# Performance work log

Measured on AMD Instinct MI355X. Metric: run time of the kernel, lower is better.

Reference implementation:

```python
import jax, jax.numpy as jnp
import numpy as np

N_NODES = 50000
N_EDGES = 1600000


def gcn_conv(x, edge_index, W, b):
    """PyG GCNConv: linear transform, add self-loops, symmetric deg^-1/2 norm, scatter-add."""
    n = x.shape[0]
    h = x @ W  # [N, out]
    loop = jnp.arange(n)
    src = jnp.concatenate([edge_index[0], loop])
    dst = jnp.concatenate([edge_index[1], loop])
    ones = jnp.ones(src.shape[0], dtype=h.dtype)
    deg = jax.ops.segment_sum(ones, dst, num_segments=n)  # in-degree incl. self-loop
    dinv = jnp.where(deg > 0, jax.lax.rsqrt(deg), 0.0)
    norm = dinv[src] * dinv[dst]  # [E+N]
    msg = h[src] * norm[:, None]  # gathered, normalized messages
    out = jax.ops.segment_sum(msg, dst, num_segments=n)
    return out + b


def setup_inputs() -> dict:
    key = jax.random.key(0)
    k1, k2, k3, k4 = jax.random.split(key, 4)
    x = jax.random.normal(k1, (N_NODES, 512), dtype=jnp.float32)
    edge_index = jax.random.randint(k2, (2, N_EDGES), 0, N_NODES, dtype=jnp.int64)
    W1 = jax.random.normal(k3, (512, 128), dtype=jnp.float32) * (1.0 / np.sqrt(512))
    b1 = jnp.zeros((128,), dtype=jnp.float32)
    W2 = jax.random.normal(k4, (128, 40), dtype=jnp.float32) * (1.0 / np.sqrt(128))
    b2 = jnp.zeros((40,), dtype=jnp.float32)
    return {"x": x, "edge_index": edge_index, "W1": W1, "b1": b1, "W2": W2, "b2": b2}


def reference(x, edge_index, W1, b1, W2, b2):
    h = gcn_conv(x, edge_index, W1, b1)
    h = jax.nn.relu(h)
    h = gcn_conv(h, edge_index, W2, b2)
    return jax.nn.log_softmax(h, axis=1)
```

## Files before the change

kernel.cpp:

```cpp
#include <hip/hip_runtime.h>
#include <hip/hip_bf16.h>
#include <math.h>


#define FEAT1 512
#define FEAT2 128
#define FEAT3 40

typedef __attribute__((ext_vector_type(8))) short bf16x8;
typedef __attribute__((ext_vector_type(4))) float f32x4;

struct __align__(16) ll2 { long long x, y; };

__device__ __forceinline__ unsigned short f2bf(float f) {
    union { float f; unsigned u; } c; c.f = f;
    unsigned r = c.u + 0x7fff + ((c.u >> 16) & 1);
    return (unsigned short)(r >> 16);
}
__device__ __forceinline__ float bf2f(unsigned v16) {
    union { unsigned u; float f; } c; c.u = v16 << 16;
    return c.f;
}

__device__ __forceinline__ bf16x8 pack_bf8(f32x4 a, f32x4 b) {
    union { __hip_bfloat162 h[4]; bf16x8 v; } u;
    u.h[0] = __float22bfloat162_rn(make_float2(a[0], a[1]));
    u.h[1] = __float22bfloat162_rn(make_float2(a[2], a[3]));
    u.h[2] = __float22bfloat162_rn(make_float2(b[0], b[1]));
    u.h[3] = __float22bfloat162_rn(make_float2(b[2], b[3]));
    return u.v;
}

__launch_bounds__(1024)
__global__ void partA_kernel(const int* __restrict__ ei,
                             int* __restrict__ gbkt, unsigned* __restrict__ part,
                             int bktCap, long E, int NB) {
    __shared__ int hist[256], lbase[256], lcur[256];
    __shared__ int anyv;
    int t = threadIdx.x;
    if (t == 0) anyv = 0;
    if (t < 256) { hist[t] = 0; lcur[t] = 0; }
    __syncthreads();
    if (t < 256 && ei[2 * t + 1] != 0) anyv = 1;
    __syncthreads();
    int f64 = (anyv == 0) ? 1 : 0;
    const long long* ei64 = (const long long*)ei;
    bool al4 = ((E & 3) == 0);

    long chunk = (E + gridDim.x - 1) / gridDim.x;
    chunk = (chunk + 3) & ~3L;
    long start = (long)blockIdx.x * chunk;
    long end = start + chunk; if (end > E) end = E;
    if (start > E) start = E;

    int srcs[8], dsts[8];
    #pragma unroll
    for (int r = 0; r < 2; r++) {
        long e0 = start + (long)r * 4096 + 4 * t;
        if (al4 && e0 + 3 < end) {
            if (f64) {
                ll2 sa = *(const ll2*)(ei64 + e0);
                ll2 sb = *(const ll2*)(ei64 + e0 + 2);
                ll2 da = *(const ll2*)(ei64 + E + e0);
                ll2 db = *(const ll2*)(ei64 + E + e0 + 2);
                srcs[4 * r + 0] = (int)sa.x; srcs[4 * r + 1] = (int)sa.y;
                srcs[4 * r + 2] = (int)sb.x; srcs[4 * r + 3] = (int)sb.y;
                dsts[4 * r + 0] = (int)da.x; dsts[4 * r + 1] = (int)da.y;
                dsts[4 * r + 2] = (int)db.x; dsts[4 * r + 3] = (int)db.y;
            } else {
                int4 s4 = *(const int4*)(ei + e0);
                int4 d4 = *(const int4*)(ei + E + e0);
                srcs[4 * r + 0] = s4.x; srcs[4 * r + 1] = s4.y;
                srcs[4 * r + 2] = s4.z; srcs[4 * r + 3] = s4.w;
                dsts[4 * r + 0] = d4.x; dsts[4 * r + 1] = d4.y;
                dsts[4 * r + 2] = d4.z; dsts[4 * r + 3] = d4.w;
            }
            #pragma unroll
            for (int u = 0; u < 4; u++) atomicAdd(&hist[dsts[4 * r + u] >> 8], 1);
        } else {
            #pragma unroll
            for (int u = 0; u < 4; u++) {
                if (e0 + u < end) {
                    if (f64) { srcs[4 * r + u] = (int)ei64[e0 + u]; dsts[4 * r + u] = (int)ei64[E + e0 + u]; }
                    else     { srcs[4 * r + u] = ei[e0 + u];        dsts[4 * r + u] = ei[E + e0 + u]; }
                    atomicAdd(&hist[dsts[4 * r + u] >> 8], 1);
                }
            }
        }
    }
    __syncthreads();
    if (t < NB && hist[t]) lbase[t] = atomicAdd(&gbkt[t], hist[t]);
    __syncthreads();

    #pragma unroll
    for (int r = 0; r < 2; r++) {
        long e0 = start + (long)r * 4096 + 4 * t;
        #pragma unroll
        for (int u = 0; u < 4; u++) {
            if (e0 + u < end) {
                int bkt = dsts[4 * r + u] >> 8;
                int pos = lbase[bkt] + atomicAdd(&lcur[bkt], 1);
                if (pos < bktCap)
                    part[(long)bkt * bktCap + pos] =
                        (unsigned)srcs[4 * r + u] | ((unsigned)(dsts[4 * r + u] & 255) << 17);
            }
        }
    }
}

__launch_bounds__(512)
__global__ void partB_kernel(const unsigned* __restrict__ part, int bktCap,
                             const int* __restrict__ gbkt,
                             int* __restrict__ offsets, float* __restrict__ dinv,
                             int* __restrict__ col, int N, int E) {
    __shared__ int h[256], sc[256], cur[256];
    int b = blockIdx.x, t = threadIdx.x;
    int NB = gridDim.x;

    if (t < 256) sc[t] = (t < NB) ? gbkt[t] : 0;
    __syncthreads();
    #pragma unroll
    for (int d = 1; d < 256; d <<= 1) {
        int tv = 0;
        if (t < 256 && t >= d) tv = sc[t - d];
        __syncthreads();
        if (t < 256) sc[t] += tv;
        __syncthreads();
    }
    int base = (b == 0) ? 0 : sc[b - 1];
    if (b == 0 && t == 0) offsets[N] = E;

    int n = gbkt[b]; if (n > bktCap) n = bktCap;
    int lo = b << 8;
    const unsigned* p = part + (long)b * bktCap;
    if (t < 256) h[t] = 0;
    __syncthreads();
    for (int i = t; i < n; i += 512) atomicAdd(&h[(p[i] >> 17) & 255], 1);
    __syncthreads();
    int cnt = (t < 256) ? h[t] : 0;
    if (t < 256) sc[t] = cnt;
    __syncthreads();
    #pragma unroll
    for (int d = 1; d < 256; d <<= 1) {
        int tv = 0;
        if (t < 256 && t >= d) tv = sc[t - d];
        __syncthreads();
        if (t < 256) sc[t] += tv;
        __syncthreads();
    }
    if (t < 256) {
        int ex = sc[t] - cnt;
        int node = lo + t;
        if (node < N) {
            offsets[node] = base + ex;
            dinv[node] = 1.0f / sqrtf((float)(cnt + 1));
        }
        cur[t] = ex;
    }
    __syncthreads();
    for (int i = t; i < n; i += 512) {
        unsigned u = p[i];
        int r = atomicAdd(&cur[(u >> 17) & 255], 1);
        col[base + r] = u & 0x1FFFF;
    }
}

__global__ void wbt_kernel(const float* __restrict__ W1, const float* __restrict__ W2,
                           unsigned short* __restrict__ Bt, unsigned short* __restrict__ Bt2,
                           int* __restrict__ gbkt) {
    int b = blockIdx.x;
    if (b == 0 && threadIdx.x < 256) gbkt[threadIdx.x] = 0;
    if (b < FEAT2) {
        int r = b, x7 = r & 7;
        for (int k = threadIdx.x; k < FEAT1; k += blockDim.x) {
            int c = k >> 3, j = k & 7;
            int eo = (((c ^ x7) << 3) | j);
            Bt[(long)r * FEAT1 + eo] = f2bf(W1[(long)k * FEAT2 + r]);
        }
    } else {
        int n = b - FEAT2;
        for (int k = threadIdx.x; k < FEAT2; k += blockDim.x)
            Bt2[(long)n * FEAT2 + k] = (n < FEAT3) ? f2bf(W2[(long)k * FEAT3 + n]) : 0;
    }
}

#define G1_NW 8
__launch_bounds__(512, 2)
__global__ void gemm1_mfma_kernel(const float* __restrict__ A,
                                  const unsigned short* __restrict__ Bsw,
                                  const float* __restrict__ dinv,
                                  unsigned short* __restrict__ C, int M) {
    __shared__ unsigned short Bl[FEAT2 * FEAT1];
    int t = threadIdx.x;

    {
        uint4 tmp[16];
        #pragma unroll
        for (int r = 0; r < 16; r++)
            tmp[r] = *(const uint4*)((const char*)Bsw + (size_t)t * 16 + (size_t)r * 8192);
        #pragma unroll
        for (int r = 0; r < 16; r++)
            *(uint4*)((char*)Bl + (size_t)t * 16 + (size_t)r * 8192) = tmp[r];
    }
    __syncthreads();

    int w = t >> 6, lane = t & 63;
    int quad = lane >> 4, r15 = lane & 15;
    int row0 = (blockIdx.x * (G1_NW * 2) + w * 2) * 16;
    int x7 = r15 & 7;

    int ar0 = row0 + r15;      if (ar0 >= M) ar0 = M - 1;
    int ar1 = row0 + 16 + r15; if (ar1 >= M) ar1 = M - 1;
    const float* ap0 = A + (long)ar0 * FEAT1 + quad * 8;
    const float* ap1 = A + (long)ar1 * FEAT1 + quad * 8;

    f32x4 ra0[3][2], ra1[3][2];
    #pragma unroll
    for (int p = 0; p < 3; p++) {
        ra0[p][0] = *(const f32x4*)(ap0 + p * 32);
        ra0[p][1] = *(const f32x4*)(ap0 + p * 32 + 4);
        ra1[p][0] = *(const f32x4*)(ap1 + p * 32);
        ra1[p][1] = *(const f32x4*)(ap1 + p * 32 + 4);
    }

    f32x4 acc0[8], acc1[8];
    #pragma unroll
    for (int nt = 0; nt < 8; nt++) {
        acc0[nt] = (f32x4){0.f, 0.f, 0.f, 0.f};
        acc1[nt] = (f32x4){0.f, 0.f, 0.f, 0.f};
    }

    #pragma unroll
    for (int ks = 0; ks < 16; ks++) {
        int sl = ks % 3;
        bf16x8 af0 = pack_bf8(ra0[sl][0], ra0[sl][1]);
        bf16x8 af1 = pack_bf8(ra1[sl][0], ra1[sl][1]);
        if (ks < 13) {
            ra0[sl][0] = *(const f32x4*)(ap0 + (ks + 3) * 32);
            ra0[sl][1] = *(const f32x4*)(ap0 + (ks + 3) * 32 + 4);
            ra1[sl][0] = *(const f32x4*)(ap1 + (ks + 3) * 32);
            ra1[sl][1] = *(const f32x4*)(ap1 + (ks + 3) * 32 + 4);
        }
        #pragma unroll
        for (int nt = 0; nt < 8; nt++) {
            int eo = (nt * 16 + r15) * FEAT1 + (((ks * 4 + quad) ^ x7) << 3);
            bf16x8 bfrag = *(const bf16x8*)(Bl + eo);
            acc0[nt] = __builtin_amdgcn_mfma_f32_16x16x32_bf16(af0, bfrag, acc0[nt], 0, 0, 0);
            acc1[nt] = __builtin_amdgcn_mfma_f32_16x16x32_bf16(af1, bfrag, acc1[nt], 0, 0, 0);
        }
    }

    #pragma unroll
    for (int tile = 0; tile < 2; tile++) {
        #pragma unroll
        for (int reg = 0; reg < 4; reg++) {
            int orow = row0 + tile * 16 + quad * 4 + reg;
            if (orow < M) {
                float di = dinv[orow];
                #pragma unroll
                for (int nt = 0; nt < 8; nt++) {
                    float v = (tile == 0) ? acc0[nt][reg] : acc1[nt][reg];
                    C[(long)orow * FEAT2 + nt * 16 + r15] = f2bf(v * di);
                }
            }
        }
    }
}

__launch_bounds__(256)
__global__ void agg1_kernel(const unsigned short* __restrict__ h1s,
                            const int* __restrict__ col, const int* __restrict__ off,
                            const float* __restrict__ dinv, const float* __restrict__ b1,
                            unsigned short* __restrict__ a1, int N, int fofs) {
    int node = blockIdx.x * 4 + (threadIdx.x >> 6);
    if (node >= N) return;
    int l = threadIdx.x & 63;
    int q = l >> 3, j = l & 7;
    const unsigned short* hp = h1s + fofs + 8 * j;
    int o0 = off[node], o1 = off[node + 1];
    float s0 = 0.f, s1 = 0.f, s2 = 0.f, s3 = 0.f,
          s4 = 0.f, s5 = 0.f, s6 = 0.f, s7 = 0.f;

    #define ACC8(P)                                                     \
        do {                                                            \
            s0 += __uint_as_float((P).x << 16);                         \
            s1 += __uint_as_float((P).x & 0xffff0000u);                 \
            s2 += __uint_as_float((P).y << 16);                         \
            s3 += __uint_as_float((P).y & 0xffff0000u);                 \
            s4 += __uint_as_float((P).z << 16);                         \
            s5 += __uint_as_float((P).z & 0xffff0000u);                 \
            s6 += __uint_as_float((P).w << 16);                         \
            s7 += __uint_as_float((P).w & 0xffff0000u);                 \
        } while (0)

    for (int base = o0; base < o1; base += 64) {
        int cnt = min(64, o1 - base);
        int myc = (l < cnt) ? col[base + l] : 0;
        int octs = cnt >> 3;
        int i = 0;
        for (; i + 4 <= octs; i += 4) {
            int c0 = __shfl(myc, 8 * i + q);
            int c1 = __shfl(myc, 8 * i + 8 + q);
            int c2 = __shfl(myc, 8 * i + 16 + q);
            int c3 = __shfl(myc, 8 * i + 24 + q);
            uint4 p0 = *(const uint4*)(hp + (long)c0 * FEAT2);
            uint4 p1 = *(const uint4*)(hp + (long)c1 * FEAT2);
            uint4 p2 = *(const uint4*)(hp + (long)c2 * FEAT2);
            uint4 p3 = *(const uint4*)(hp + (long)c3 * FEAT2);
            ACC8(p0); ACC8(p1); ACC8(p2); ACC8(p3);
        }
        for (; i < octs; ++i) {
            int c0 = __shfl(myc, 8 * i + q);
            uint4 p0 = *(const uint4*)(hp + (long)c0 * FEAT2);
            ACC8(p0);
        }
        int e = (octs << 3) + q;
        int ct = __shfl(myc, e);
        if (e < cnt) {
            uint4 p0 = *(const uint4*)(hp + (long)ct * FEAT2);
            ACC8(p0);
        }
    }
    #undef ACC8

    s0 += __shfl_xor(s0, 8);  s1 += __shfl_xor(s1, 8);
    s2 += __shfl_xor(s2, 8);  s3 += __shfl_xor(s3, 8);
    s4 += __shfl_xor(s4, 8);  s5 += __shfl_xor(s5, 8);
    s6 += __shfl_xor(s6, 8);  s7 += __shfl_xor(s7, 8);
    s0 += __shfl_xor(s0, 16); s1 += __shfl_xor(s1, 16);
    s2 += __shfl_xor(s2, 16); s3 += __shfl_xor(s3, 16);
    s4 += __shfl_xor(s4, 16); s5 += __shfl_xor(s5, 16);
    s6 += __shfl_xor(s6, 16); s7 += __shfl_xor(s7, 16);
    s0 += __shfl_xor(s0, 32); s1 += __shfl_xor(s1, 32);
    s2 += __shfl_xor(s2, 32); s3 += __shfl_xor(s3, 32);
    s4 += __shfl_xor(s4, 32); s5 += __shfl_xor(s5, 32);
    s6 += __shfl_xor(s6, 32); s7 += __shfl_xor(s7, 32);

    if (l < 8) {
        uint4 pv = *(const uint4*)(hp + (long)node * FEAT2);
        s0 += __uint_as_float(pv.x << 16); s1 += __uint_as_float(pv.x & 0xffff0000u);
        s2 += __uint_as_float(pv.y << 16); s3 += __uint_as_float(pv.y & 0xffff0000u);
        s4 += __uint_as_float(pv.z << 16); s5 += __uint_as_float(pv.z & 0xffff0000u);
        s6 += __uint_as_float(pv.w << 16); s7 += __uint_as_float(pv.w & 0xffff0000u);
        float di = dinv[node];
        float4 ba = *(const float4*)(b1 + fofs + 8 * j);
        float4 bb = *(const float4*)(b1 + fofs + 8 * j + 4);
        float v0 = s0 * di + ba.x, v1 = s1 * di + ba.y;
        float v2 = s2 * di + ba.z, v3 = s3 * di + ba.w;
        float v4 = s4 * di + bb.x, v5 = s5 * di + bb.y;
        float v6 = s6 * di + bb.z, v7 = s7 * di + bb.w;
        v0 = v0 > 0.f ? v0 : 0.f; v1 = v1 > 0.f ? v1 : 0.f;
        v2 = v2 > 0.f ? v2 : 0.f; v3 = v3 > 0.f ? v3 : 0.f;
        v4 = v4 > 0.f ? v4 : 0.f; v5 = v5 > 0.f ? v5 : 0.f;
        v6 = v6 > 0.f ? v6 : 0.f; v7 = v7 > 0.f ? v7 : 0.f;
        uint4 o;
        o.x = (unsigned)f2bf(v0) | ((unsigned)f2bf(v1) << 16);
        o.y = (unsigned)f2bf(v2) | ((unsigned)f2bf(v3) << 16);
        o.z = (unsigned)f2bf(v4) | ((unsigned)f2bf(v5) << 16);
        o.w = (unsigned)f2bf(v6) | ((unsigned)f2bf(v7) << 16);
        *(uint4*)(a1 + (long)node * FEAT2 + fofs + 8 * j) = o;
    }
}

__launch_bounds__(256)
__global__ void gemm2_mfma_kernel(const unsigned short* __restrict__ A,
                                  const unsigned short* __restrict__ Bt2,
                                  const float* __restrict__ dinv,
                                  unsigned short* __restrict__ C, int M) {
    int wave = blockIdx.x * (blockDim.x >> 6) + (threadIdx.x >> 6);
    int lane = threadIdx.x & 63;
    int quad = lane >> 4, r15 = lane & 15;
    int row0 = wave * 16;
    if (row0 >= M) return;
    int arow = row0 + r15;
    if (arow >= M) arow = M - 1;

    bf16x8 af[4];
    const unsigned short* ap = A + (long)arow * FEAT2 + quad * 8;
    #pragma unroll
    for (int ks = 0; ks < 4; ks++) af[ks] = *(const bf16x8*)(ap + ks * 32);

    f32x4 acc[3];
    #pragma unroll
    for (int nt = 0; nt < 3; nt++) acc[nt] = (f32x4){0.f, 0.f, 0.f, 0.f};
    #pragma unroll
    for (int ks = 0; ks < 4; ks++) {
        #pragma unroll
        for (int nt = 0; nt < 3; nt++) {
            bf16x8 bf = *(const bf16x8*)(Bt2 + (long)(nt * 16 + r15) * FEAT2 + ks * 32 + quad * 8);
            acc[nt] = __builtin_amdgcn_mfma_f32_16x16x32_bf16(af[ks], bf, acc[nt], 0, 0, 0);
        }
    }

    #pragma unroll
    for (int reg = 0; reg < 4; reg++) {
        int orow = row0 + quad * 4 + reg;
        if (orow >= M) continue;
        float di = dinv[orow];
        #pragma unroll
        for (int nt = 0; nt < 3; nt++) {
            int ocol = nt * 16 + r15;
            if (ocol < FEAT3)
                C[(long)orow * FEAT3 + ocol] = f2bf(acc[nt][reg] * di);
        }
    }
}

__launch_bounds__(256)
__global__ void agg2_lsm_kernel(const unsigned short* __restrict__ h2s,
                                const int* __restrict__ col, const int* __restrict__ off,
                                const float* __restrict__ dinv, const float* __restrict__ b2,
                                float* __restrict__ out, int N) {
    int node = blockIdx.x * 4 + (threadIdx.x >> 6);
    if (node >= N) return;
    int l = threadIdx.x & 63;
    int q = l >> 4, jj = l & 15;
    bool act = jj < 10;
    const unsigned short* hp = h2s + 4 * jj;
    int o0 = off[node], o1 = off[node + 1];
    float s0 = 0.f, s1 = 0.f, s2 = 0.f, s3 = 0.f;

    #define ACC4(P)                                                     \
        do {                                                            \
            s0 += __uint_as_float((P).x << 16);                         \
            s1 += __uint_as_float((P).x & 0xffff0000u);                 \
            s2 += __uint_as_float((P).y << 16);                         \
            s3 += __uint_as_float((P).y & 0xffff0000u);                 \
        } while (0)

    for (int base = o0; base < o1; base += 64) {
        int cnt = min(64, o1 - base);
        int myc = (l < cnt) ? col[base + l] : 0;
        int quads = cnt >> 2;
        int i = 0;
        for (; i + 4 <= quads; i += 4) {
            int c0 = __shfl(myc, 4 * i + q);
            int c1 = __shfl(myc, 4 * i + 4 + q);
            int c2 = __shfl(myc, 4 * i + 8 + q);
            int c3 = __shfl(myc, 4 * i + 12 + q);
            if (act) {
                uint2 p0 = *(const uint2*)(hp + (long)c0 * FEAT3);
                uint2 p1 = *(const uint2*)(hp + (long)c1 * FEAT3);
                uint2 p2 = *(const uint2*)(hp + (long)c2 * FEAT3);
                uint2 p3 = *(const uint2*)(hp + (long)c3 * FEAT3);
                ACC4(p0); ACC4(p1); ACC4(p2); ACC4(p3);
            }
        }
        for (; i < quads; ++i) {
            int c0 = __shfl(myc, 4 * i + q);
            if (act) {
                uint2 p0 = *(const uint2*)(hp + (long)c0 * FEAT3);
                ACC4(p0);
            }
        }
        int e = (quads << 2) + q;
        int ct = __shfl(myc, e);
        if (e < cnt && act) {
            uint2 p0 = *(const uint2*)(hp + (long)ct * FEAT3);
            ACC4(p0);
        }
    }
    #undef ACC4

    s0 += __shfl_xor(s0, 16); s1 += __shfl_xor(s1, 16);
    s2 += __shfl_xor(s2, 16); s3 += __shfl_xor(s3, 16);
    s0 += __shfl_xor(s0, 32); s1 += __shfl_xor(s1, 32);
    s2 += __shfl_xor(s2, 32); s3 += __shfl_xor(s3, 32);

    float v0 = -INFINITY, v1 = -INFINITY, v2 = -INFINITY, v3 = -INFINITY;
    if (act) {
        uint2 pv = *(const uint2*)(hp + (long)node * FEAT3);
        s0 += __uint_as_float(pv.x << 16); s1 += __uint_as_float(pv.x & 0xffff0000u);
        s2 += __uint_as_float(pv.y << 16); s3 += __uint_as_float(pv.y & 0xffff0000u);
        float di = dinv[node];
        float4 b = *(const float4*)(b2 + 4 * jj);
        v0 = s0 * di + b.x; v1 = s1 * di + b.y;
        v2 = s2 * di + b.z; v3 = s3 * di + b.w;
    }
    float m = fmaxf(fmaxf(v0, v1), fmaxf(v2, v3));
    #pragma unroll
    for (int o = 1; o < 16; o <<= 1) m = fmaxf(m, __shfl_xor(m, o));
    float e = act ? (expf(v0 - m) + expf(v1 - m) + expf(v2 - m) + expf(v3 - m)) : 0.f;
    #pragma unroll
    for (int o = 1; o < 16; o <<= 1) e += __shfl_xor(e, o);
    float ls = logf(e);
    if (q == 0 && act) {
        *(float4*)(out + (long)node * FEAT3 + 4 * jj) =
            make_float4(v0 - m - ls, v1 - m - ls, v2 - m - ls, v3 - m - ls);
    }
}

extern "C" void kernel_launch(void* const* d_in, const int* in_sizes, int n_in,
                              void* d_out, int out_size, void* d_ws, size_t ws_size,
                              hipStream_t stream) {
    const float* x  = (const float*)d_in[0];
    const int*   ei = (const int*)d_in[1];
    const float* W1 = (const float*)d_in[2];
    const float* b1 = (const float*)d_in[3];
    const float* W2 = (const float*)d_in[4];
    const float* b2 = (const float*)d_in[5];
    float* out = (float*)d_out;

    const int  N = in_sizes[0] / FEAT1;
    const long E = in_sizes[1] / 2;

    char* ws = (char*)d_ws;
    size_t off = 0;
    auto alloc = [&](size_t bytes) -> void* {
        off = (off + 255) & ~(size_t)255;
        void* p = ws + off;
        off += bytes;
        return p;
    };
    const int NB = (N + 255) >> 8;
    const int bktCap = (int)(E / NB) + 1024;
    int*   offsets = (int*)alloc((size_t)(N + 1) * 4);
    float* dinv    = (float*)alloc((size_t)N * 4);
    int*   col     = (int*)alloc((size_t)E * 4);
    unsigned short* h1s = (unsigned short*)alloc((size_t)N * FEAT2 * 2);
    unsigned short* a1  = (unsigned short*)alloc((size_t)N * FEAT2 * 2);
    unsigned short* h2s = (unsigned short*)alloc((size_t)N * FEAT3 * 2);
    unsigned short* Bt  = (unsigned short*)alloc((size_t)FEAT2 * FEAT1 * 2);
    unsigned short* Bt2 = (unsigned short*)alloc((size_t)48 * FEAT2 * 2);
    unsigned* part = (unsigned*)alloc((size_t)NB * bktCap * 4);
    int*   gbkt    = (int*)alloc(256 * 4);

    wbt_kernel<<<176, 256, 0, stream>>>(W1, W2, Bt, Bt2, gbkt);
    partA_kernel<<<256, 1024, 0, stream>>>(ei, gbkt, part, bktCap, E, NB);
    partB_kernel<<<NB, 512, 0, stream>>>(part, bktCap, gbkt, offsets, dinv, col, N, (int)E);
    {
        int tiles  = (N + 15) / 16;
        int blocks = (tiles + G1_NW * 2 - 1) / (G1_NW * 2);
        gemm1_mfma_kernel<<<blocks, 512, 0, stream>>>(x, Bt, dinv, h1s, N);
    }
    agg1_kernel<<<(N + 3) / 4, 256, 0, stream>>>(h1s, col, offsets, dinv, b1, a1, N, 0);
    agg1_kernel<<<(N + 3) / 4, 256, 0, stream>>>(h1s, col, offsets, dinv, b1, a1, N, 64);
    gemm2_mfma_kernel<<<(N / 16 + 3) / 4, 256, 0, stream>>>(a1, Bt2, dinv, h2s, N);
    agg2_lsm_kernel<<<(N + 3) / 4, 256, 0, stream>>>(h2s, col, offsets, dinv, b2, out, N);
}
```

Baseline: 303.9 us.

## Store h1 in four 32-column slabs and aggregate in four passes

The first GEMM now writes its bf16 output as four contiguous 32-feature slabs (N x 32 each) instead of row-major N x 128. The layer-1 aggregation runs four passes, one per slab, with 4 lanes per neighbour row and 16 neighbours gathered at once. Each pass's gather working set is smaller (3.2 MB instead of 6.4 MB for the old half-width passes), so it is more likely to stay in L2/cache. In exchange there are more kernel launches, the col array is re-read four times, and each gather is a 64-byte row segment.

```diff
diff --git a/kernel.cpp b/kernel.cpp
--- a/kernel.cpp
+++ b/kernel.cpp
@@ -260,7 +260,8 @@
                 #pragma unroll
                 for (int nt = 0; nt < 8; nt++) {
                     float v = (tile == 0) ? acc0[nt][reg] : acc1[nt][reg];
-                    C[(long)orow * FEAT2 + nt * 16 + r15] = f2bf(v * di);
+                    C[(size_t)(nt >> 1) * M * 32 + (long)orow * 32 + ((nt & 1) << 4) + r15] =
+                        f2bf(v * di);
                 }
             }
         }
@@ -268,15 +269,15 @@
 }
 
 __launch_bounds__(256)
-__global__ void agg1_kernel(const unsigned short* __restrict__ h1s,
+__global__ void agg1_kernel(const unsigned short* __restrict__ h1q,
                             const int* __restrict__ col, const int* __restrict__ off,
                             const float* __restrict__ dinv, const float* __restrict__ b1,
-                            unsigned short* __restrict__ a1, int N, int fofs) {
+                            unsigned short* __restrict__ a1, int N, int pass) {
     int node = blockIdx.x * 4 + (threadIdx.x >> 6);
     if (node >= N) return;
     int l = threadIdx.x & 63;
-    int q = l >> 3, j = l & 7;
-    const unsigned short* hp = h1s + fofs + 8 * j;
+    int q = l >> 2, j = l & 3;
+    const unsigned short* hp = h1q + (size_t)pass * N * 32 + 8 * j;
     int o0 = off[node], o1 = off[node + 1];
     float s0 = 0.f, s1 = 0.f, s2 = 0.f, s3 = 0.f,
           s4 = 0.f, s5 = 0.f, s6 = 0.f, s7 = 0.f;
@@ -296,33 +297,33 @@
     for (int base = o0; base < o1; base += 64) {
         int cnt = min(64, o1 - base);
         int myc = (l < cnt) ? col[base + l] : 0;
-        int octs = cnt >> 3;
+        int steps = cnt >> 4;
         int i = 0;
-        for (; i + 4 <= octs; i += 4) {
-            int c0 = __shfl(myc, 8 * i + q);
-            int c1 = __shfl(myc, 8 * i + 8 + q);
-            int c2 = __shfl(myc, 8 * i + 16 + q);
-            int c3 = __shfl(myc, 8 * i + 24 + q);
-            uint4 p0 = *(const uint4*)(hp + (long)c0 * FEAT2);
-            uint4 p1 = *(const uint4*)(hp + (long)c1 * FEAT2);
-            uint4 p2 = *(const uint4*)(hp + (long)c2 * FEAT2);
-            uint4 p3 = *(const uint4*)(hp + (long)c3 * FEAT2);
-            ACC8(p0); ACC8(p1); ACC8(p2); ACC8(p3);
-        }
-        for (; i < octs; ++i) {
-            int c0 = __shfl(myc, 8 * i + q);
-            uint4 p0 = *(const uint4*)(hp + (long)c0 * FEAT2);
+        for (; i + 2 <= steps; i += 2) {
+            int c0 = __shfl(myc, 16 * i + q);
+            int c1 = __shfl(myc, 16 * i + 16 + q);
+            uint4 p0 = *(const uint4*)(hp + (long)c0 * 32);
+            uint4 p1 = *(const uint4*)(hp + (long)c1 * 32);
+            ACC8(p0); ACC8(p1);
+        }
+        for (; i < steps; ++i) {
+            int c0 = __shfl(myc, 16 * i + q);
+            uint4 p0 = *(const uint4*)(hp + (long)c0 * 32);
             ACC8(p0);
         }
-        int e = (octs << 3) + q;
+        int e = (steps << 4) + q;
         int ct = __shfl(myc, e);
         if (e < cnt) {
-            uint4 p0 = *(const uint4*)(hp + (long)ct * FEAT2);
+            uint4 p0 = *(const uint4*)(hp + (long)ct * 32);
             ACC8(p0);
         }
     }
     #undef ACC8
 
+    s0 += __shfl_xor(s0, 4);  s1 += __shfl_xor(s1, 4);
+    s2 += __shfl_xor(s2, 4);  s3 += __shfl_xor(s3, 4);
+    s4 += __shfl_xor(s4, 4);  s5 += __shfl_xor(s5, 4);
+    s6 += __shfl_xor(s6, 4);  s7 += __shfl_xor(s7, 4);
     s0 += __shfl_xor(s0, 8);  s1 += __shfl_xor(s1, 8);
     s2 += __shfl_xor(s2, 8);  s3 += __shfl_xor(s3, 8);
     s4 += __shfl_xor(s4, 8);  s5 += __shfl_xor(s5, 8);
@@ -336,15 +337,16 @@
     s4 += __shfl_xor(s4, 32); s5 += __shfl_xor(s5, 32);
     s6 += __shfl_xor(s6, 32); s7 += __shfl_xor(s7, 32);
 
-    if (l < 8) {
-        uint4 pv = *(const uint4*)(hp + (long)node * FEAT2);
+    if (l < 4) {
+        uint4 pv = *(const uint4*)(hp + (long)node * 32);
         s0 += __uint_as_float(pv.x << 16); s1 += __uint_as_float(pv.x & 0xffff0000u);
         s2 += __uint_as_float(pv.y << 16); s3 += __uint_as_float(pv.y & 0xffff0000u);
         s4 += __uint_as_float(pv.z << 16); s5 += __uint_as_float(pv.z & 0xffff0000u);
         s6 += __uint_as_float(pv.w << 16); s7 += __uint_as_float(pv.w & 0xffff0000u);
         float di = dinv[node];
-        float4 ba = *(const float4*)(b1 + fofs + 8 * j);
-        float4 bb = *(const float4*)(b1 + fofs + 8 * j + 4);
+        int fofs = pass * 32 + 8 * j;
+        float4 ba = *(const float4*)(b1 + fofs);
+        float4 bb = *(const float4*)(b1 + fofs + 4);
         float v0 = s0 * di + ba.x, v1 = s1 * di + ba.y;
         float v2 = s2 * di + ba.z, v3 = s3 * di + ba.w;
         float v4 = s4 * di + bb.x, v5 = s5 * di + bb.y;
@@ -358,7 +360,7 @@
         o.y = (unsigned)f2bf(v2) | ((unsigned)f2bf(v3) << 16);
         o.z = (unsigned)f2bf(v4) | ((unsigned)f2bf(v5) << 16);
         o.w = (unsigned)f2bf(v6) | ((unsigned)f2bf(v7) << 16);
-        *(uint4*)(a1 + (long)node * FEAT2 + fofs + 8 * j) = o;
+        *(uint4*)(a1 + (long)node * FEAT2 + fofs) = o;
     }
 }
 
@@ -517,7 +519,7 @@
     int*   offsets = (int*)alloc((size_t)(N + 1) * 4);
     float* dinv    = (float*)alloc((size_t)N * 4);
     int*   col     = (int*)alloc((size_t)E * 4);
-    unsigned short* h1s = (unsigned short*)alloc((size_t)N * FEAT2 * 2);
+    unsigned short* h1q = (unsigned short*)alloc((size_t)N * FEAT2 * 2);
     unsigned short* a1  = (unsigned short*)alloc((size_t)N * FEAT2 * 2);
     unsigned short* h2s = (unsigned short*)alloc((size_t)N * FEAT3 * 2);
     unsigned short* Bt  = (unsigned short*)alloc((size_t)FEAT2 * FEAT1 * 2);
@@ -531,10 +533,10 @@
     {
         int tiles  = (N + 15) / 16;
         int blocks = (tiles + G1_NW * 2 - 1) / (G1_NW * 2);
-        gemm1_mfma_kernel<<<blocks, 512, 0, stream>>>(x, Bt, dinv, h1s, N);
-    }
-    agg1_kernel<<<(N + 3) / 4, 256, 0, stream>>>(h1s, col, offsets, dinv, b1, a1, N, 0);
-    agg1_kernel<<<(N + 3) / 4, 256, 0, stream>>>(h1s, col, offsets, dinv, b1, a1, N, 64);
+        gemm1_mfma_kernel<<<blocks, 512, 0, stream>>>(x, Bt, dinv, h1q, N);
+    }
+    for (int pass = 0; pass < 4; pass++)
+        agg1_kernel<<<(N + 3) / 4, 256, 0, stream>>>(h1q, col, offsets, dinv, b1, a1, N, pass);
     gemm2_mfma_kernel<<<(N / 16 + 3) / 4, 256, 0, stream>>>(a1, Bt2, dinv, h2s, N);
     agg2_lsm_kernel<<<(N + 3) / 4, 256, 0, stream>>>(h2s, col, offsets, dinv, b2, out, N);
 }
```

New measurement: 347.2 us. 1.14x slower.
